# Kernel optimization log

Hardware: AMD Instinct MI355X
Metric: run time of the kernel (lower is better)

## Reference

```python
import jax, jax.numpy as jnp
import numpy as np

B_SZ, T_A, T_B, EMB, HID = 16, 1024, 1024, 768, 1024

def setup_inputs() -> dict:
    key = jax.random.key(0)
    kA, kB, k1, k2 = jax.random.split(key, 4)
    s1 = 1.0 / np.sqrt(EMB)
    s2 = 1.0 / np.sqrt(HID)
    return {
        "A": jax.random.normal(kA, (B_SZ, T_A, EMB), jnp.float32),
        "B": jax.random.normal(kB, (B_SZ, T_B, EMB), jnp.float32),
        "W1": jax.random.normal(k1, (EMB, HID), jnp.float32) * s1,
        "b1": jnp.zeros((HID,), jnp.float32),
        "W2": jax.random.normal(k2, (HID, HID), jnp.float32) * s2,
        "b2": jnp.zeros((HID,), jnp.float32),
    }

def _mlp(x, W1, b1, W2, b2):
    # Linear -> ReLU -> Linear -> ReLU (dropout omitted / eval mode)
    h = jax.nn.relu(x @ W1 + b1)
    return jax.nn.relu(h @ W2 + b2)

def reference(A, B, W1, b1, W2, b2):
    f_A = _mlp(A, W1, b1, W2, b2)             # (bs, ta, h)
    f_B = _mlp(B, W1, b1, W2, b2)             # (bs, tb, h)
    e = jnp.einsum("bah,bch->bac", f_A, f_B)  # (bs, ta, tb)
    beta = jnp.einsum("bac,bce->bae", jax.nn.softmax(e, axis=-1), B)
    alpha = jnp.einsum("bca,bae->bce",
                       jax.nn.softmax(e, axis=1).transpose(0, 2, 1)[:, :, :] * 1.0,
                       A) if False else jnp.einsum(
        "bca,bae->bce", jax.nn.softmax(e.transpose(0, 2, 1), axis=-1), A)
    return beta, alpha
```

## Files before the change

### kernel.cpp

```cpp
#include <hip/hip_runtime.h>
#include <cstdint>


#define L2E 1.4426950408889634f

typedef _Float16 half8 __attribute__((ext_vector_type(8)));
typedef _Float16 half4v __attribute__((ext_vector_type(4)));
typedef float f32x4 __attribute__((ext_vector_type(4)));

__device__ __forceinline__ void gl_lds16(const void* g, void* l) {
  __builtin_amdgcn_global_load_lds(
      (const __attribute__((address_space(1))) unsigned int*)g,
      (__attribute__((address_space(3))) unsigned int*)l, 16, 0, 0);
}

template<int K, bool BIASRELU, bool STATS, typename OutT>
__global__ __launch_bounds__(256, 2)
void gemm_k(const _Float16* __restrict__ X, const _Float16* __restrict__ Y,
            const float* __restrict__ bias, OutT* __restrict__ C, int N,
            long xbs, long ybs, long cbs, int gm, int gn, int gz,
            float* __restrict__ prm, float* __restrict__ prs,
            float* __restrict__ pcm, float* __restrict__ pcs,
            const _Float16* __restrict__ X2, const _Float16* __restrict__ Y2,
            OutT* __restrict__ C2, int shalf)
{
  __shared__ __align__(16) _Float16 sA[128 * 64];
  __shared__ __align__(16) _Float16 sB[128 * 64];
  const int t = threadIdx.x;
  const int lane = t & 63, w = t >> 6;
  const int wr = w >> 1, wc = w & 1;
  const int lm = lane & 15, g = lane >> 4;
  const int xr = lane & 7;

  const int id = blockIdx.x;
  const int c = id & 7;
  int s = id >> 3;
  if (shalf && s >= shalf) { s -= shalf; X = X2; Y = Y2; C = C2; }
  int m, n, bz;
  if (gz == 1) {
    int q = s / gn;
    n = s - q * gn;
    m = c * (gm >> 3) + q;
    bz = 0;
  } else {
    int tpb = gm * gn;
    int bq = s / tpb;
    bz = c * (gz >> 3) + bq;
    int r = s - bq * tpb;
    m = r / gn;
    n = r - m * gn;
  }
  const int m0 = m * 128, n0 = n * 128;

  X += (size_t)bz * xbs;
  Y += (size_t)bz * ybs;
  C += (size_t)bz * cbs;

  const int stg_row = t >> 3;
  const int stg_koff = (((t & 7) ^ ((t >> 3) & 7)) << 3);

  int arow[4], brow[4], axo[2];
#pragma unroll
  for (int i = 0; i < 4; ++i) {
    arow[i] = (wr * 64 + i * 16 + lm) * 64;
    brow[i] = (wc * 64 + i * 16 + lm) * 64;
  }
  axo[0] = ((0 * 4 + g) ^ xr) * 8;
  axo[1] = ((1 * 4 + g) ^ xr) * 8;

  f32x4 acc[4][4] = {};

  for (int kt = 0; kt < K; kt += 64) {
    __syncthreads();
#pragma unroll
    for (int r = 0; r < 4; ++r) {
      int row = r * 32 + stg_row;
      gl_lds16(X + (size_t)(m0 + row) * K + kt + stg_koff, sA + (r * 256 + t) * 8);
    }
#pragma unroll
    for (int r = 0; r < 4; ++r) {
      int row = r * 32 + stg_row;
      gl_lds16(Y + (size_t)(n0 + row) * K + kt + stg_koff, sB + (r * 256 + t) * 8);
    }
    __syncthreads();

    half8 af[4], bf[4];
#pragma unroll
    for (int ks = 0; ks < 2; ++ks) {
#pragma unroll
      for (int mi = 0; mi < 4; ++mi)
        af[mi] = *(const half8*)(sA + arow[mi] + axo[ks]);
#pragma unroll
      for (int ni = 0; ni < 4; ++ni)
        bf[ni] = *(const half8*)(sB + brow[ni] + axo[ks]);
#pragma unroll
      for (int mi = 0; mi < 4; ++mi)
#pragma unroll
        for (int ni = 0; ni < 4; ++ni)
          acc[mi][ni] = __builtin_amdgcn_mfma_f32_16x16x32_f16(af[mi], bf[ni], acc[mi][ni], 0, 0, 0);
    }
  }

#pragma unroll
  for (int mi = 0; mi < 4; ++mi) {
    const int rbase = m0 + wr * 64 + mi * 16 + (lane >> 4) * 4;
#pragma unroll
    for (int ni = 0; ni < 4; ++ni) {
      const int col = n0 + wc * 64 + ni * 16 + lm;
      float bv = 0.f;
      if constexpr (BIASRELU) bv = bias[col];
#pragma unroll
      for (int q = 0; q < 4; ++q) {
        float v = acc[mi][ni][q] + bv;
        if constexpr (BIASRELU) v = fmaxf(v, 0.f);
        C[(size_t)(rbase + q) * N + col] = (OutT)v;
      }
    }
  }

  if constexpr (STATS) {
    __shared__ float sRm[256], sRs[256], sCm[256], sCs[256];
    float rowm[4][4], rows_[4][4];
#pragma unroll
    for (int mi = 0; mi < 4; ++mi) {
#pragma unroll
      for (int q = 0; q < 4; ++q) {
        float mloc = fmaxf(fmaxf(acc[mi][0][q], acc[mi][1][q]),
                           fmaxf(acc[mi][2][q], acc[mi][3][q]));
#pragma unroll
        for (int msk = 1; msk < 16; msk <<= 1)
          mloc = fmaxf(mloc, __shfl_xor(mloc, msk));
        float sl = 0.f;
#pragma unroll
        for (int ni = 0; ni < 4; ++ni)
          sl += exp2f((acc[mi][ni][q] - mloc) * L2E);
#pragma unroll
        for (int msk = 1; msk < 16; msk <<= 1)
          sl += __shfl_xor(sl, msk);
        rowm[mi][q] = mloc;
        rows_[mi][q] = sl;
      }
    }
    if (lm == 0) {
#pragma unroll
      for (int mi = 0; mi < 4; ++mi)
#pragma unroll
        for (int q = 0; q < 4; ++q) {
          int rloc = wr * 64 + mi * 16 + (lane >> 4) * 4 + q;
          sRm[wc * 128 + rloc] = rowm[mi][q];
          sRs[wc * 128 + rloc] = rows_[mi][q];
        }
    }
#pragma unroll
    for (int ni = 0; ni < 4; ++ni) {
      float mloc = -3.0e38f;
#pragma unroll
      for (int mi = 0; mi < 4; ++mi)
#pragma unroll
        for (int q = 0; q < 4; ++q)
          mloc = fmaxf(mloc, acc[mi][ni][q]);
      mloc = fmaxf(mloc, __shfl_xor(mloc, 16));
      mloc = fmaxf(mloc, __shfl_xor(mloc, 32));
      float sl = 0.f;
#pragma unroll
      for (int mi = 0; mi < 4; ++mi)
#pragma unroll
        for (int q = 0; q < 4; ++q)
          sl += exp2f((acc[mi][ni][q] - mloc) * L2E);
      sl += __shfl_xor(sl, 16);
      sl += __shfl_xor(sl, 32);
      if ((lane >> 4) == 0) {
        int cloc = wc * 64 + ni * 16 + lm;
        sCm[wr * 128 + cloc] = mloc;
        sCs[wr * 128 + cloc] = sl;
      }
    }
    __syncthreads();
    if (t < 128) {
      float m1 = sRm[t], m2 = sRm[128 + t];
      float M = fmaxf(m1, m2);
      float S = sRs[t] * exp2f((m1 - M) * L2E) + sRs[128 + t] * exp2f((m2 - M) * L2E);
      size_t o = ((size_t)bz * 8 + n) * 1024 + m0 + t;
      prm[o] = M;
      prs[o] = S;
    } else {
      int u = t - 128;
      float m1 = sCm[u], m2 = sCm[128 + u];
      float M = fmaxf(m1, m2);
      float S = sCs[u] * exp2f((m1 - M) * L2E) + sCs[128 + u] * exp2f((m2 - M) * L2E);
      size_t o = ((size_t)bz * 8 + m) * 1024 + n0 + u;
      pcm[o] = M;
      pcs[o] = S;
    }
  }
}

__global__ __launch_bounds__(256)
void softmax_apply(const float* __restrict__ e,
                   const float* __restrict__ prm, const float* __restrict__ prs,
                   const float* __restrict__ pcm, const float* __restrict__ pcs,
                   _Float16* __restrict__ P, _Float16* __restrict__ PT)
{
  __shared__ _Float16 tl[64][65];
  __shared__ float sRm[64], sRi[64], sCm[64], sCi[64];
  const int bz = blockIdx.z;
  const int r0 = blockIdx.y * 64, c0 = blockIdx.x * 64;
  const size_t bo = (size_t)bz * 1048576;
  const int t = threadIdx.x;

  if (t < 128) {
    const int isCol = t >> 6;
    const int u = t & 63;
    const float* pm = isCol ? pcm : prm;
    const float* ps = isCol ? pcs : prs;
    const int pos = (isCol ? c0 : r0) + u;
    float mj[8], sj[8];
#pragma unroll
    for (int j = 0; j < 8; ++j) {
      size_t o = ((size_t)bz * 8 + j) * 1024 + pos;
      mj[j] = pm[o];
      sj[j] = ps[o];
    }
    float M = -3.0e38f;
#pragma unroll
    for (int j = 0; j < 8; ++j) M = fmaxf(M, mj[j]);
    float S = 0.f;
#pragma unroll
    for (int j = 0; j < 8; ++j) S += sj[j] * exp2f((mj[j] - M) * L2E);
    if (isCol) { sCm[u] = M; sCi[u] = 1.f / S; }
    else       { sRm[u] = M; sRi[u] = 1.f / S; }
  }
  __syncthreads();

#pragma unroll
  for (int p = 0; p < 4; ++p) {
    int idx = p * 256 + t;
    int row = idx >> 4, col4 = (idx & 15) * 4;
    float4 v = *(const float4*)(e + bo + (size_t)(r0 + row) * 1024 + c0 + col4);
    float vv[4] = {v.x, v.y, v.z, v.w};
    const float mrow = sRm[row];
    const float irow = sRi[row];
    half4v op;
#pragma unroll
    for (int j = 0; j < 4; ++j) {
      op[j] = (_Float16)(exp2f((vv[j] - mrow) * L2E) * irow);
      tl[col4 + j][row] = (_Float16)(exp2f((vv[j] - sCm[col4 + j]) * L2E) * sCi[col4 + j]);
    }
    *(half4v*)(P + bo + (size_t)(r0 + row) * 1024 + c0 + col4) = op;
  }
  __syncthreads();
#pragma unroll
  for (int p = 0; p < 4; ++p) {
    int idx = p * 256 + t;
    int trow = idx >> 4, tcol4 = (idx & 15) * 4;
    half4v ov;
#pragma unroll
    for (int j = 0; j < 4; ++j) ov[j] = tl[trow][tcol4 + j];
    *(half4v*)(PT + bo + (size_t)(c0 + trow) * 1024 + r0 + tcol4) = ov;
  }
}

__global__ __launch_bounds__(256)
void transpose_cvt(const float* __restrict__ in1, _Float16* __restrict__ out1,
                   const float* __restrict__ in2, _Float16* __restrict__ out2,
                   int R, int C, int nb)
{
  __shared__ float tl[32][33];
  int z = blockIdx.z;
  const float* in = in1;
  _Float16* out = out1;
  if (z >= nb) { z -= nb; in = in2; out = out2; }
  const size_t bo = (size_t)z * R * C;
  int x = blockIdx.x * 32 + threadIdx.x;
  int y0 = blockIdx.y * 32;
  for (int i = threadIdx.y; i < 32; i += 8)
    tl[i][threadIdx.x] = in[bo + (size_t)(y0 + i) * C + x];
  __syncthreads();
  int xo = y0 + threadIdx.x;
  int c0 = blockIdx.x * 32;
  for (int i = threadIdx.y; i < 32; i += 8)
    out[bo + (size_t)(c0 + i) * R + xo] = (_Float16)tl[threadIdx.x][i];
}

__global__ __launch_bounds__(256)
void cvt_f16_2(const float* __restrict__ inA, const float* __restrict__ inB,
               _Float16* __restrict__ oA, _Float16* __restrict__ oB, int n4)
{
  int i = blockIdx.x * 256 + threadIdx.x;
  const float* in = inA;
  _Float16* out = oA;
  if (i >= n4) { i -= n4; in = inB; out = oB; }
  float4 v = ((const float4*)in)[i];
  half4v o;
  o[0] = (_Float16)v.x; o[1] = (_Float16)v.y; o[2] = (_Float16)v.z; o[3] = (_Float16)v.w;
  ((half4v*)out)[i] = o;
}

extern "C" void kernel_launch(void* const* d_in, const int* in_sizes, int n_in,
                              void* d_out, int out_size, void* d_ws, size_t ws_size,
                              hipStream_t stream)
{
  const float* A  = (const float*)d_in[0];
  const float* B  = (const float*)d_in[1];
  const float* W1 = (const float*)d_in[2];
  const float* b1 = (const float*)d_in[3];
  const float* W2 = (const float*)d_in[4];
  const float* b2 = (const float*)d_in[5];
  float* out = (float*)d_out;

  char* ws = (char*)d_ws;
  _Float16* Af  = (_Float16*)(ws + 0);
  _Float16* Bf  = (_Float16*)(ws + 25165824);
  _Float16* W1t = (_Float16*)(ws + 50331648);
  _Float16* W2t = (_Float16*)(ws + 51904512);
  float*    prm = (float*)   (ws + 50331648);
  float*    prs = (float*)   (ws + 50331648 + 524288);
  float*    pcm = (float*)   (ws + 50331648 + 1048576);
  float*    pcs = (float*)   (ws + 50331648 + 1572864);
  _Float16* fAB = (_Float16*)(ws + 54001664);
  _Float16* P   = (_Float16*)(ws + 54001664);
  _Float16* PT  = (_Float16*)(ws + 87556096);
  _Float16* h   = (_Float16*)(ws + 121110528);
  float*    e   = (float*)   (ws + 121110528);
  _Float16* fA = fAB;
  _Float16* fB = fAB + 16777216;
  _Float16* At = Af;
  _Float16* Bt = Bf;

  dim3 blk(256);
  dim3 tblk(32, 8);

  cvt_f16_2<<<24576, blk, 0, stream>>>(A, B, Af, Bf, 3145728);
  transpose_cvt<<<dim3(32, 24, 1), tblk, 0, stream>>>(W1, W1t, nullptr, nullptr, 768, 1024, 1);
  transpose_cvt<<<dim3(32, 32, 1), tblk, 0, stream>>>(W2, W2t, nullptr, nullptr, 1024, 1024, 1);

  gemm_k<768, true, false, _Float16><<<2048, blk, 0, stream>>>(
      Af, W1t, b1, h, 1024, 0, 0, 0, 256, 8, 1,
      nullptr, nullptr, nullptr, nullptr, nullptr, nullptr, nullptr, 0);
  transpose_cvt<<<dim3(24, 32, 32), tblk, 0, stream>>>(A, At, B, Bt, 1024, 768, 16);
  gemm_k<1024, true, false, _Float16><<<2048, blk, 0, stream>>>(
      h, W2t, b2, fAB, 1024, 0, 0, 0, 256, 8, 1,
      nullptr, nullptr, nullptr, nullptr, nullptr, nullptr, nullptr, 0);

  gemm_k<1024, false, true, float><<<1024, blk, 0, stream>>>(
      fA, fB, nullptr, e, 1024, 1048576L, 1048576L, 1048576L, 8, 8, 16,
      prm, prs, pcm, pcs, nullptr, nullptr, nullptr, 0);

  softmax_apply<<<dim3(16, 16, 16), blk, 0, stream>>>(e, prm, prs, pcm, pcs, P, PT);

  gemm_k<1024, false, false, float><<<1536, blk, 0, stream>>>(
      P, Bt, nullptr, out, 768, 1048576L, 786432L, 786432L, 8, 6, 16,
      nullptr, nullptr, nullptr, nullptr, PT, At, out + 12582912, 96);
}
```

Before: 514.9 us.

## Enlarge GEMM tiles to 256x256 with 512 threads and a 4-stage LDS pipeline

The GEMM kernel now uses 256x256 output tiles computed by 8 waves, with K split into 32-wide steps and a 4-buffer asynchronous global-to-LDS pipeline that is three stages deep. Loads for future stages are issued while MFMAs run, vmcnt waits replace full syncthreads, and setprio raises wave priority around the MFMA blocks. The aim is more data reuse per tile and hidden memory latency. In exchange, grids shrink to 256-512 blocks, which may underfill the CUs, and the 128KB of LDS plus the larger accumulators limit occupancy. Softmax partial stats now use 4 tiles per dimension instead of 8.

```diff
diff --git a/kernel.cpp b/kernel.cpp
--- a/kernel.cpp
+++ b/kernel.cpp
@@ -15,7 +15,7 @@
 }
 
 template<int K, bool BIASRELU, bool STATS, typename OutT>
-__global__ __launch_bounds__(256, 2)
+__global__ __launch_bounds__(512, 2)
 void gemm_k(const _Float16* __restrict__ X, const _Float16* __restrict__ Y,
             const float* __restrict__ bias, OutT* __restrict__ C, int N,
             long xbs, long ybs, long cbs, int gm, int gn, int gz,
@@ -24,86 +24,105 @@
             const _Float16* __restrict__ X2, const _Float16* __restrict__ Y2,
             OutT* __restrict__ C2, int shalf)
 {
-  __shared__ __align__(16) _Float16 sA[128 * 64];
-  __shared__ __align__(16) _Float16 sB[128 * 64];
+  constexpr int NS = K / 32;
+  __shared__ __align__(16) _Float16 sm[65536];
   const int t = threadIdx.x;
   const int lane = t & 63, w = t >> 6;
-  const int wr = w >> 1, wc = w & 1;
+  const int wr = w >> 2, wc = w & 3;
   const int lm = lane & 15, g = lane >> 4;
-  const int xr = lane & 7;
 
   const int id = blockIdx.x;
   const int c = id & 7;
-  int s = id >> 3;
-  if (shalf && s >= shalf) { s -= shalf; X = X2; Y = Y2; C = C2; }
+  int s0 = id >> 3;
+  if (shalf && s0 >= shalf) { s0 -= shalf; X = X2; Y = Y2; C = C2; }
   int m, n, bz;
   if (gz == 1) {
-    int q = s / gn;
-    n = s - q * gn;
+    int q = s0 / gn;
+    n = s0 - q * gn;
     m = c * (gm >> 3) + q;
     bz = 0;
   } else {
     int tpb = gm * gn;
-    int bq = s / tpb;
+    int bq = s0 / tpb;
     bz = c * (gz >> 3) + bq;
-    int r = s - bq * tpb;
+    int r = s0 - bq * tpb;
     m = r / gn;
     n = r - m * gn;
   }
-  const int m0 = m * 128, n0 = n * 128;
+  const int m0 = m * 256, n0 = n * 256;
 
   X += (size_t)bz * xbs;
   Y += (size_t)bz * ybs;
   C += (size_t)bz * cbs;
 
-  const int stg_row = t >> 3;
-  const int stg_koff = (((t & 7) ^ ((t >> 3) & 7)) << 3);
-
-  int arow[4], brow[4], axo[2];
-#pragma unroll
-  for (int i = 0; i < 4; ++i) {
-    arow[i] = (wr * 64 + i * 16 + lm) * 64;
-    brow[i] = (wc * 64 + i * 16 + lm) * 64;
-  }
-  axo[0] = ((0 * 4 + g) ^ xr) * 8;
-  axo[1] = ((1 * 4 + g) ^ xr) * 8;
-
-  f32x4 acc[4][4] = {};
-
-  for (int kt = 0; kt < K; kt += 64) {
-    __syncthreads();
-#pragma unroll
-    for (int r = 0; r < 4; ++r) {
-      int row = r * 32 + stg_row;
-      gl_lds16(X + (size_t)(m0 + row) * K + kt + stg_koff, sA + (r * 256 + t) * 8);
-    }
-#pragma unroll
-    for (int r = 0; r < 4; ++r) {
-      int row = r * 32 + stg_row;
-      gl_lds16(Y + (size_t)(n0 + row) * K + kt + stg_koff, sB + (r * 256 + t) * 8);
-    }
-    __syncthreads();
-
-    half8 af[4], bf[4];
-#pragma unroll
-    for (int ks = 0; ks < 2; ++ks) {
-#pragma unroll
-      for (int mi = 0; mi < 4; ++mi)
-        af[mi] = *(const half8*)(sA + arow[mi] + axo[ks]);
-#pragma unroll
-      for (int ni = 0; ni < 4; ++ni)
-        bf[ni] = *(const half8*)(sB + brow[ni] + axo[ks]);
-#pragma unroll
-      for (int mi = 0; mi < 4; ++mi)
-#pragma unroll
-        for (int ni = 0; ni < 4; ++ni)
-          acc[mi][ni] = __builtin_amdgcn_mfma_f32_16x16x32_f16(af[mi], bf[ni], acc[mi][ni], 0, 0, 0);
-    }
-  }
-
-#pragma unroll
-  for (int mi = 0; mi < 4; ++mi) {
-    const int rbase = m0 + wr * 64 + mi * 16 + (lane >> 4) * 4;
+  const _Float16* ag[2]; const _Float16* bg[2];
+  _Float16* al[2]; _Float16* bl[2];
+#pragma unroll
+  for (int j = 0; j < 2; ++j) {
+    int ci = j * 512 + t;
+    int lr = ci >> 3, p = ci & 7;
+    int cc = p ^ (lr & 7);
+    int r = lr * 2 + (cc >> 2);
+    int kb = (cc & 3) * 8;
+    ag[j] = X + (size_t)(m0 + r) * K + kb;
+    bg[j] = Y + (size_t)(n0 + r) * K + kb;
+    al[j] = sm + ci * 8;
+    bl[j] = sm + 8192 + ci * 8;
+  }
+
+  int aoff[8], boff[4];
+#pragma unroll
+  for (int mi = 0; mi < 8; ++mi) {
+    int r = wr * 128 + mi * 16 + lm;
+    int lr = r >> 1;
+    aoff[mi] = lr * 64 + ((((lm & 1) << 2) + g) ^ (lr & 7)) * 8;
+  }
+#pragma unroll
+  for (int ni = 0; ni < 4; ++ni) {
+    int r = wc * 64 + ni * 16 + lm;
+    int lr = r >> 1;
+    boff[ni] = lr * 64 + ((((lm & 1) << 2) + g) ^ (lr & 7)) * 8;
+  }
+
+  f32x4 acc[8][4] = {};
+
+#define STAGE_(ss) { \
+    const int sb_ = ((ss) & 3) * 16384; \
+    const int kt_ = (ss) * 32; \
+    gl_lds16(ag[0] + kt_, al[0] + sb_); \
+    gl_lds16(ag[1] + kt_, al[1] + sb_); \
+    gl_lds16(bg[0] + kt_, bl[0] + sb_); \
+    gl_lds16(bg[1] + kt_, bl[1] + sb_); }
+
+#define SLOT_(ss, VM) { \
+    asm volatile("s_waitcnt vmcnt(" #VM ")" ::: "memory"); \
+    __builtin_amdgcn_s_barrier(); \
+    const _Float16* ab_ = sm + ((ss) & 3) * 16384; \
+    const _Float16* bb_ = ab_ + 8192; \
+    half8 af[8]; half8 bf[4]; \
+    _Pragma("unroll") \
+    for (int mi = 0; mi < 8; ++mi) af[mi] = *(const half8*)(ab_ + aoff[mi]); \
+    _Pragma("unroll") \
+    for (int ni = 0; ni < 4; ++ni) bf[ni] = *(const half8*)(bb_ + boff[ni]); \
+    if ((ss) + 3 < NS) STAGE_((ss) + 3); \
+    __builtin_amdgcn_s_setprio(1); \
+    _Pragma("unroll") \
+    for (int mi = 0; mi < 8; ++mi) \
+      _Pragma("unroll") \
+      for (int ni = 0; ni < 4; ++ni) \
+        acc[mi][ni] = __builtin_amdgcn_mfma_f32_16x16x32_f16(af[mi], bf[ni], acc[mi][ni], 0, 0, 0); \
+    __builtin_amdgcn_s_setprio(0); }
+
+  STAGE_(0); STAGE_(1); STAGE_(2);
+  for (int ss = 0; ss < NS - 2; ++ss) SLOT_(ss, 8);
+  SLOT_(NS - 2, 4);
+  SLOT_(NS - 1, 0);
+#undef STAGE_
+#undef SLOT_
+
+#pragma unroll
+  for (int mi = 0; mi < 8; ++mi) {
+    const int rb = m0 + wr * 128 + mi * 16 + g * 4;
 #pragma unroll
     for (int ni = 0; ni < 4; ++ni) {
       const int col = n0 + wc * 64 + ni * 16 + lm;
@@ -113,16 +132,20 @@
       for (int q = 0; q < 4; ++q) {
         float v = acc[mi][ni][q] + bv;
         if constexpr (BIASRELU) v = fmaxf(v, 0.f);
-        C[(size_t)(rbase + q) * N + col] = (OutT)v;
+        C[(size_t)(rb + q) * N + col] = (OutT)v;
       }
     }
   }
 
   if constexpr (STATS) {
-    __shared__ float sRm[256], sRs[256], sCm[256], sCs[256];
-    float rowm[4][4], rows_[4][4];
-#pragma unroll
-    for (int mi = 0; mi < 4; ++mi) {
+    __syncthreads();
+    float* sRm = (float*)sm;
+    float* sRs = sRm + 1024;
+    float* sCm = sRs + 1024;
+    float* sCs = sCm + 512;
+
+#pragma unroll
+    for (int mi = 0; mi < 8; ++mi) {
 #pragma unroll
       for (int q = 0; q < 4; ++q) {
         float mloc = fmaxf(fmaxf(acc[mi][0][q], acc[mi][1][q]),
@@ -137,25 +160,18 @@
 #pragma unroll
         for (int msk = 1; msk < 16; msk <<= 1)
           sl += __shfl_xor(sl, msk);
-        rowm[mi][q] = mloc;
-        rows_[mi][q] = sl;
+        if (lm == 0) {
+          int r = wr * 128 + mi * 16 + g * 4 + q;
+          sRm[wc * 256 + r] = mloc;
+          sRs[wc * 256 + r] = sl;
+        }
       }
-    }
-    if (lm == 0) {
-#pragma unroll
-      for (int mi = 0; mi < 4; ++mi)
-#pragma unroll
-        for (int q = 0; q < 4; ++q) {
-          int rloc = wr * 64 + mi * 16 + (lane >> 4) * 4 + q;
-          sRm[wc * 128 + rloc] = rowm[mi][q];
-          sRs[wc * 128 + rloc] = rows_[mi][q];
-        }
     }
 #pragma unroll
     for (int ni = 0; ni < 4; ++ni) {
       float mloc = -3.0e38f;
 #pragma unroll
-      for (int mi = 0; mi < 4; ++mi)
+      for (int mi = 0; mi < 8; ++mi)
 #pragma unroll
         for (int q = 0; q < 4; ++q)
           mloc = fmaxf(mloc, acc[mi][ni][q]);
@@ -163,32 +179,36 @@
       mloc = fmaxf(mloc, __shfl_xor(mloc, 32));
       float sl = 0.f;
 #pragma unroll
-      for (int mi = 0; mi < 4; ++mi)
+      for (int mi = 0; mi < 8; ++mi)
 #pragma unroll
         for (int q = 0; q < 4; ++q)
           sl += exp2f((acc[mi][ni][q] - mloc) * L2E);
       sl += __shfl_xor(sl, 16);
       sl += __shfl_xor(sl, 32);
-      if ((lane >> 4) == 0) {
-        int cloc = wc * 64 + ni * 16 + lm;
-        sCm[wr * 128 + cloc] = mloc;
-        sCs[wr * 128 + cloc] = sl;
+      if (g == 0) {
+        int cl = wc * 64 + ni * 16 + lm;
+        sCm[wr * 256 + cl] = mloc;
+        sCs[wr * 256 + cl] = sl;
       }
     }
     __syncthreads();
-    if (t < 128) {
-      float m1 = sRm[t], m2 = sRm[128 + t];
-      float M = fmaxf(m1, m2);
-      float S = sRs[t] * exp2f((m1 - M) * L2E) + sRs[128 + t] * exp2f((m2 - M) * L2E);
-      size_t o = ((size_t)bz * 8 + n) * 1024 + m0 + t;
+    if (t < 256) {
+      float M = sRm[t];
+#pragma unroll
+      for (int j = 1; j < 4; ++j) M = fmaxf(M, sRm[j * 256 + t]);
+      float S = 0.f;
+#pragma unroll
+      for (int j = 0; j < 4; ++j)
+        S += sRs[j * 256 + t] * exp2f((sRm[j * 256 + t] - M) * L2E);
+      size_t o = ((size_t)bz * 4 + n) * 1024 + m0 + t;
       prm[o] = M;
       prs[o] = S;
     } else {
-      int u = t - 128;
-      float m1 = sCm[u], m2 = sCm[128 + u];
-      float M = fmaxf(m1, m2);
-      float S = sCs[u] * exp2f((m1 - M) * L2E) + sCs[128 + u] * exp2f((m2 - M) * L2E);
-      size_t o = ((size_t)bz * 8 + m) * 1024 + n0 + u;
+      int u = t - 256;
+      float M = fmaxf(sCm[u], sCm[256 + u]);
+      float S = sCs[u] * exp2f((sCm[u] - M) * L2E) +
+                sCs[256 + u] * exp2f((sCm[256 + u] - M) * L2E);
+      size_t o = ((size_t)bz * 4 + m) * 1024 + n0 + u;
       pcm[o] = M;
       pcs[o] = S;
     }
@@ -214,19 +234,19 @@
     const float* pm = isCol ? pcm : prm;
     const float* ps = isCol ? pcs : prs;
     const int pos = (isCol ? c0 : r0) + u;
-    float mj[8], sj[8];
-#pragma unroll
-    for (int j = 0; j < 8; ++j) {
-      size_t o = ((size_t)bz * 8 + j) * 1024 + pos;
+    float mj[4], sj[4];
+#pragma unroll
+    for (int j = 0; j < 4; ++j) {
+      size_t o = ((size_t)bz * 4 + j) * 1024 + pos;
       mj[j] = pm[o];
       sj[j] = ps[o];
     }
     float M = -3.0e38f;
 #pragma unroll
-    for (int j = 0; j < 8; ++j) M = fmaxf(M, mj[j]);
+    for (int j = 0; j < 4; ++j) M = fmaxf(M, mj[j]);
     float S = 0.f;
 #pragma unroll
-    for (int j = 0; j < 8; ++j) S += sj[j] * exp2f((mj[j] - M) * L2E);
+    for (int j = 0; j < 4; ++j) S += sj[j] * exp2f((mj[j] - M) * L2E);
     if (isCol) { sCm[u] = M; sCi[u] = 1.f / S; }
     else       { sRm[u] = M; sRi[u] = 1.f / S; }
   }
@@ -328,27 +348,28 @@
   _Float16* Bt = Bf;
 
   dim3 blk(256);
+  dim3 blk5(512);
   dim3 tblk(32, 8);
 
   cvt_f16_2<<<24576, blk, 0, stream>>>(A, B, Af, Bf, 3145728);
   transpose_cvt<<<dim3(32, 24, 1), tblk, 0, stream>>>(W1, W1t, nullptr, nullptr, 768, 1024, 1);
   transpose_cvt<<<dim3(32, 32, 1), tblk, 0, stream>>>(W2, W2t, nullptr, nullptr, 1024, 1024, 1);
 
-  gemm_k<768, true, false, _Float16><<<2048, blk, 0, stream>>>(
-      Af, W1t, b1, h, 1024, 0, 0, 0, 256, 8, 1,
+  gemm_k<768, true, false, _Float16><<<512, blk5, 0, stream>>>(
+      Af, W1t, b1, h, 1024, 0, 0, 0, 128, 4, 1,
       nullptr, nullptr, nullptr, nullptr, nullptr, nullptr, nullptr, 0);
   transpose_cvt<<<dim3(24, 32, 32), tblk, 0, stream>>>(A, At, B, Bt, 1024, 768, 16);
-  gemm_k<1024, true, false, _Float16><<<2048, blk, 0, stream>>>(
-      h, W2t, b2, fAB, 1024, 0, 0, 0, 256, 8, 1,
+  gemm_k<1024, true, false, _Float16><<<512, blk5, 0, stream>>>(
+      h, W2t, b2, fAB, 1024, 0, 0, 0, 128, 4, 1,
       nullptr, nullptr, nullptr, nullptr, nullptr, nullptr, nullptr, 0);
 
-  gemm_k<1024, false, true, float><<<1024, blk, 0, stream>>>(
-      fA, fB, nullptr, e, 1024, 1048576L, 1048576L, 1048576L, 8, 8, 16,
+  gemm_k<1024, false, true, float><<<256, blk5, 0, stream>>>(
+      fA, fB, nullptr, e, 1024, 1048576L, 1048576L, 1048576L, 4, 4, 16,
       prm, prs, pcm, pcs, nullptr, nullptr, nullptr, 0);
 
   softmax_apply<<<dim3(16, 16, 16), blk, 0, stream>>>(e, prm, prs, pcm, pcs, P, PT);
 
-  gemm_k<1024, false, false, float><<<1536, blk, 0, stream>>>(
-      P, Bt, nullptr, out, 768, 1048576L, 786432L, 786432L, 8, 6, 16,
-      nullptr, nullptr, nullptr, nullptr, PT, At, out + 12582912, 96);
-}
+  gemm_k<1024, false, false, float><<<384, blk5, 0, stream>>>(
+      P, Bt, nullptr, out, 768, 1048576L, 786432L, 786432L, 4, 3, 16,
+      nullptr, nullptr, nullptr, nullptr, PT, At, out + 12582912, 24);
+}
```

After: 508.9 us. Within noise of the previous version (-1.2%).
